# Kernel optimization log

Measured on AMD Instinct MI355X. Metric: run time of the kernel, lower is better.

## Reference

```python
import jax, jax.numpy as jnp
import numpy as np

N = 100000
K = 8
DK = 16          # d_in/K == d_out/K
E = 1600000
EPS = 1e-12      # torch F.normalize eps


def setup_inputs() -> dict:
    key = jax.random.key(0)
    k1, k2, k3, k4 = jax.random.split(key, 4)
    f_in = jax.random.normal(k1, (N, K, DK), dtype=jnp.float32)
    Ep = jax.random.randint(k2, (E, 2), 0, N, dtype=jnp.int64)
    En = jax.random.randint(k3, (E, 2), 0, N, dtype=jnp.int64)
    # xavier_uniform over (K, 5*DK, DK): fan_in=5*DK, fan_out=DK
    limit = float(np.sqrt(6.0 / (5 * DK + DK)))
    W = jax.random.uniform(k4, (K, 5 * DK, DK), dtype=jnp.float32,
                           minval=-limit, maxval=limit)
    b = jnp.zeros((1, K, DK), dtype=jnp.float32)
    return {"f_in": f_in, "Ep": Ep, "En": En, "W": W, "b": b}


def _aggregate(Ep, En, f_in):
    n = f_in.shape[0]
    seg = lambda vals, idx: jax.ops.segment_sum(vals, idx, num_segments=n)
    m_p_out = seg(f_in[Ep[:, 1]], Ep[:, 0])
    m_p_in = seg(f_in[Ep[:, 0]], Ep[:, 1])
    m_n_out = seg(f_in[En[:, 1]], En[:, 0])
    m_n_in = seg(f_in[En[:, 0]], En[:, 1])
    return m_p_out, m_p_in, m_n_out, m_n_in


def reference(f_in, Ep, En, W, b):
    m_p_out, m_p_in, m_n_out, m_n_in = _aggregate(Ep, En, f_in)
    # (N, K, 5*DK)
    m_concat = jnp.concatenate([m_p_out, m_p_in, f_in, m_n_out, m_n_in], axis=2)
    # per-factor grouped matmul: (N,K,5DK) x (K,5DK,DK) -> (N,K,DK)
    f_out = jnp.einsum('nkf,kfo->nko', m_concat, W) + b
    a = jnp.tanh(f_out)
    # F.normalize: L2 over dim=1 (factor axis), clamp_min eps
    norm = jnp.maximum(jnp.linalg.norm(a, axis=1, keepdims=True), EPS)
    return a / norm
```

## Files before the change

kernel.cpp:

```cpp
#include <hip/hip_runtime.h>
#include <math.h>


#define ROW 128
#define ROW4 32
#define BC   256
#define BSH  8

__device__ __forceinline__ void push_entry(
    int* __restrict__ cnt, int* __restrict__ ovfCnt, int* __restrict__ ovf,
    int* __restrict__ idxbuf, int seg, int src, int PAD, int ovfCap)
{
    int slot = atomicAdd(&cnt[seg], 1);
    if (slot < PAD) {
        idxbuf[(size_t)seg * PAD + slot] = src;
    } else {
        int oi = atomicAdd(ovfCnt, 1);
        if (oi < ovfCap) { ovf[2*oi] = seg; ovf[2*oi+1] = src; }
    }
}

__global__ __launch_bounds__(256) void fill_kernel(
    const int4* __restrict__ Ep2, const int4* __restrict__ En2,
    const int* __restrict__ Ep, const int* __restrict__ En,
    int* __restrict__ cnt, int* __restrict__ ovfCnt, int* __restrict__ ovf,
    int* __restrict__ idxbuf, int Epairs, int Etail, int N, int PAD, int ovfCap)
{
    int i = blockIdx.x * 256 + threadIdx.x;
    int stride = gridDim.x * 256;
    for (int e = i; e < Epairs; e += stride) {
        int4 p = Ep2[e];
        push_entry(cnt, ovfCnt, ovf, idxbuf, 4*p.x + 0, p.y, PAD, ovfCap);
        push_entry(cnt, ovfCnt, ovf, idxbuf, 4*p.y + 1, p.x, PAD, ovfCap);
        push_entry(cnt, ovfCnt, ovf, idxbuf, 4*p.z + 0, p.w, PAD, ovfCap);
        push_entry(cnt, ovfCnt, ovf, idxbuf, 4*p.w + 1, p.z, PAD, ovfCap);
        int4 q = En2[e];
        push_entry(cnt, ovfCnt, ovf, idxbuf, 4*q.x + 2, q.y, PAD, ovfCap);
        push_entry(cnt, ovfCnt, ovf, idxbuf, 4*q.y + 3, q.x, PAD, ovfCap);
        push_entry(cnt, ovfCnt, ovf, idxbuf, 4*q.z + 2, q.w, PAD, ovfCap);
        push_entry(cnt, ovfCnt, ovf, idxbuf, 4*q.w + 3, q.z, PAD, ovfCap);
    }
    if (i == 0 && Etail) {
        int e = 2 * Epairs;
        int a = Ep[2*e], b = Ep[2*e+1];
        push_entry(cnt, ovfCnt, ovf, idxbuf, 4*a + 0, b, PAD, ovfCap);
        push_entry(cnt, ovfCnt, ovf, idxbuf, 4*b + 1, a, PAD, ovfCap);
        int c = En[2*e], d = En[2*e+1];
        push_entry(cnt, ovfCnt, ovf, idxbuf, 4*c + 2, d, PAD, ovfCap);
        push_entry(cnt, ovfCnt, ovf, idxbuf, 4*d + 3, c, PAD, ovfCap);
    }
}

__global__ __launch_bounds__(256) void fill_bucket(
    const int4* __restrict__ Ep2, const int4* __restrict__ En2,
    const int* __restrict__ Ep, const int* __restrict__ En,
    int* __restrict__ cnt2, int* __restrict__ cells,
    int* __restrict__ ovfCnt, int* __restrict__ ovf,
    int Epairs, int Etail, int B, int CAP, int ovfCap)
{
    __shared__ int lcnt[1024];
    const int w = blockIdx.x;
    int* __restrict__ mycell = cells + (size_t)w * B * CAP;

    for (int i = threadIdx.x; i < 1024; i += 256) lcnt[i] = 0;
    __syncthreads();

    auto pushB = [&](int dst, int l, int src) {
        int bkt  = dst >> BSH;
        int slot = atomicAdd(&lcnt[bkt], 1);
        if (slot < CAP) {
            mycell[(size_t)bkt * CAP + slot] =
                src | ((dst & (BC - 1)) << 17) | (l << 25);
        } else {
            int oi = atomicAdd(ovfCnt, 1);
            if (oi < ovfCap) { ovf[2*oi] = 4*dst + l; ovf[2*oi+1] = src; }
        }
    };

    int stride = gridDim.x * 256;
    for (int e = blockIdx.x * 256 + threadIdx.x; e < Epairs; e += stride) {
        int4 p = Ep2[e];
        pushB(p.x, 0, p.y); pushB(p.y, 1, p.x);
        pushB(p.z, 0, p.w); pushB(p.w, 1, p.z);
        int4 q = En2[e];
        pushB(q.x, 2, q.y); pushB(q.y, 3, q.x);
        pushB(q.z, 2, q.w); pushB(q.w, 3, q.z);
    }
    if (w == 0 && threadIdx.x == 0 && Etail) {
        int e = 2 * Epairs;
        int a = Ep[2*e], b = Ep[2*e+1];
        pushB(a, 0, b); pushB(b, 1, a);
        int c = En[2*e], d = En[2*e+1];
        pushB(c, 2, d); pushB(d, 3, c);
    }
    __syncthreads();
    for (int b = threadIdx.x; b < B; b += 256) {
        int v = lcnt[b];
        cnt2[(size_t)w * B + b] = (v < CAP) ? v : CAP;
    }
}

__global__ __launch_bounds__(512) void build_csr(
    const int* __restrict__ cnt2, const int* __restrict__ cells,
    int* __restrict__ cnt, int* __restrict__ idxbuf,
    int* __restrict__ ovfCnt, int* __restrict__ ovf,
    int N, int B, int CAP, int PAD, int WN, int ovfCap)
{
    __shared__ int scnt[4 * BC];
    const int b = blockIdx.x;
    const int nodeBase = b << BSH;

    for (int i = threadIdx.x; i < 4 * BC; i += 512) scnt[i] = 0;
    __syncthreads();

    auto proc = [&](int p) {
        int src  = p & 0x1FFFF;
        int dl   = (p >> 17) & (BC - 1);
        int l    = (p >> 25) & 3;
        int segl = (dl << 2) | l;
        int slot = atomicAdd(&scnt[segl], 1);
        if (slot < PAD) {
            idxbuf[(size_t)((nodeBase + dl) * 4 + l) * PAD + slot] = src;
        } else {
            int oi = atomicAdd(ovfCnt, 1);
            if (oi < ovfCap) {
                ovf[2*oi] = (nodeBase + dl) * 4 + l; ovf[2*oi+1] = src;
            }
        }
    };

    for (int w = threadIdx.x; w < WN; w += 512) {
        int c = cnt2[(size_t)w * B + b];
        const int4* __restrict__ cell4 =
            (const int4*)(cells + ((size_t)w * B + b) * CAP);
        for (int i = 0; i < c; i += 4) {
            int4 v = cell4[i >> 2];
            proc(v.x);
            if (i + 1 < c) proc(v.y);
            if (i + 2 < c) proc(v.z);
            if (i + 3 < c) proc(v.w);
        }
    }
    __syncthreads();
    for (int i = threadIdx.x; i < 4 * BC; i += 512) {
        int node = nodeBase + (i >> 2);
        if (node < N) cnt[node * 4 + (i & 3)] = scnt[i];
    }
}

__global__ __launch_bounds__(128) void ovf_zero(
    const int* __restrict__ ovfCnt, const int* __restrict__ ovf,
    float* __restrict__ out, int* __restrict__ nflag, int ovfCap)
{
    const int t = threadIdx.x;
    int nOv = *ovfCnt;
    if (nOv > ovfCap) nOv = ovfCap;
    for (int i = blockIdx.x; i < nOv; i += gridDim.x) {
        int dst = ovf[2*i] >> 2;
        out[(size_t)dst*ROW + t] = 0.f;
        if (t == 0) nflag[dst] = 1;
    }
}

__global__ __launch_bounds__(256) void ovf_kernel(
    const float* __restrict__ f_in, const float* __restrict__ W,
    const int* __restrict__ ovfCnt, const int* __restrict__ ovf,
    float* __restrict__ out, int N, int ovfCap)
{
    const int t = threadIdx.x & 127;
    const int k = t >> 4;
    const int o = t & 15;
    int nOv = *ovfCnt;
    if (nOv > ovfCap) nOv = ovfCap;
    const int group  = blockIdx.x * 2 + (threadIdx.x >> 7);
    const int stride = gridDim.x * 2;
    for (int i = group; i < nOv; i += stride) {
        int seg = ovf[2*i], src = ovf[2*i+1];
        int l = seg & 3;
        int dst = seg >> 2;
        int s = (l < 2) ? l : l + 1;
        float y = 0.f;
#pragma unroll
        for (int ii = 0; ii < 16; ++ii)
            y += f_in[(size_t)src*ROW + k*16 + ii] * W[k*1280 + (s*16 + ii)*16 + o];
        unsafeAtomicAdd(&out[(size_t)dst*ROW + t], y);
    }
}

__global__ __launch_bounds__(256, 4) void pull_kernel(
    const float4* __restrict__ f_in4,
    const float*  __restrict__ f_in,
    const int*    __restrict__ cnt,
    const int*    __restrict__ idxbuf,
    const float*  __restrict__ W,
    const float*  __restrict__ bias,
    const int*    __restrict__ ovfCnt,
    const int*    __restrict__ nflag,
    float*        __restrict__ out,
    int nStart, int nEnd, int PAD)
{
    __shared__ float4 sacc4[2][5][ROW4];
    __shared__ float  syp[2][ROW];
    __shared__ float  sa[ROW];

    const int tid  = threadIdx.x;
    const int elem = tid & 127;
    const int h    = tid >> 7;
    const int k    = elem >> 4;
    const int o    = elem & 15;
    const int oct  = tid >> 5;
    const int l    = oct >> 1;
    const int hh   = oct & 1;
    const int e4   = tid & 31;
    const int slot = (l < 2) ? l : l + 1;

    float w[5][8];
#pragma unroll
    for (int s = 0; s < 5; ++s)
#pragma unroll
        for (int i = 0; i < 8; ++i)
            w[s][i] = W[k*1280 + (s*16 + h*8 + i)*16 + o];
    const float bb = bias[elem];
    const int haveOvf = *ovfCnt;

    for (int n = nStart + blockIdx.x; n < nEnd; n += gridDim.x) {
        float pre = 0.f;
        if (h == 0 && haveOvf)
            pre = nflag[n] ? out[(size_t)n*ROW + elem] : 0.f;

        int c = cnt[4*n + l];
        if (c > PAD) c = PAD;
        const size_t base = (size_t)(4*n + l) * PAD;
        const int mid = (c + 1) >> 1;
        int j         = hh ? mid : 0;
        const int end = hh ? c   : mid;

        float4 acc = make_float4(0.f, 0.f, 0.f, 0.f);
        for (; j + 3 < end; j += 4) {
            int j0 = idxbuf[base + j],     j1 = idxbuf[base + j + 1];
            int j2 = idxbuf[base + j + 2], j3 = idxbuf[base + j + 3];
            float4 r0 = f_in4[(size_t)j0*ROW4 + e4];
            float4 r1 = f_in4[(size_t)j1*ROW4 + e4];
            float4 r2 = f_in4[(size_t)j2*ROW4 + e4];
            float4 r3 = f_in4[(size_t)j3*ROW4 + e4];
            acc.x += r0.x + r1.x + r2.x + r3.x;
            acc.y += r0.y + r1.y + r2.y + r3.y;
            acc.z += r0.z + r1.z + r2.z + r3.z;
            acc.w += r0.w + r1.w + r2.w + r3.w;
        }
        for (; j < end; ++j) {
            float4 r = f_in4[(size_t)idxbuf[base + j]*ROW4 + e4];
            acc.x += r.x; acc.y += r.y; acc.z += r.z; acc.w += r.w;
        }
        sacc4[hh][slot][e4] = acc;
        if (oct == 0) sacc4[0][2][e4] = f_in4[(size_t)n*ROW4 + e4];
        if (oct == 1) sacc4[1][2][e4] = make_float4(0.f, 0.f, 0.f, 0.f);
        __syncthreads();

        float y = 0.f;
#pragma unroll
        for (int s = 0; s < 5; ++s) {
            const float* m0 = (const float*)&sacc4[0][s][0] + k*16 + h*8;
            const float* m1 = (const float*)&sacc4[1][s][0] + k*16 + h*8;
#pragma unroll
            for (int i = 0; i < 8; ++i)
                y += (m0[i] + m1[i]) * w[s][i];
        }
        syp[h][elem] = y;
        __syncthreads();

        float a = 0.f;
        if (h == 0) {
            a = tanhf(syp[0][elem] + syp[1][elem] + bb + pre);
            sa[elem] = a;
        }
        __syncthreads();
        if (h == 0) {
            float ss = 0.f;
#pragma unroll
            for (int k2 = 0; k2 < 8; ++k2) {
                float v = sa[k2*16 + o];
                ss += v * v;
            }
            out[(size_t)n*ROW + elem] = a / fmaxf(sqrtf(ss), 1e-12f);
        }
        __syncthreads();
    }
}

extern "C" void kernel_launch(void* const* d_in, const int* in_sizes, int n_in,
                              void* d_out, int out_size, void* d_ws, size_t ws_size,
                              hipStream_t stream) {
    const float* f_in = (const float*)d_in[0];
    const int*   Ep   = (const int*)d_in[1];
    const int*   En   = (const int*)d_in[2];
    const float* W    = (const float*)d_in[3];
    const float* b    = (const float*)d_in[4];
    float* out = (float*)d_out;

    const int N = in_sizes[0] / ROW;
    const int E = in_sizes[1] / 2;
    const int Epairs = E / 2;
    const int Etail  = E & 1;
    const int M = 4 * N;
    const int B = (N + BC - 1) / BC;
    const int Nh = N >> 1;

    bool newpath = (N <= 131072) && (B <= 1024);
    int PAD = 0, CAP = 0, WN = 0;
    if (newpath) {
        const int cfg1k[][2]  = {{48,32},{40,32},{32,32},{32,24},{24,24},
                                 {24,16},{16,16}};
        const int cfg512[][2] = {{64,48},{48,48},{48,40},{40,40},{40,32},
                                 {32,32},{32,24},{24,24},{16,16}};
        const int wnl[2] = {1024, 512};
        for (int wi = 0; wi < 2 && !WN; ++wi) {
            int wn = wnl[wi];
            const int (*cfg)[2] = wi ? cfg512 : cfg1k;
            int ncfg = wi ? 9 : 7;
            for (int i = 0; i < ncfg; ++i) {
                int pad = cfg[i][0], cap = cfg[i][1];
                size_t need = ((size_t)M + 64 + N + (size_t)wn * B
                               + (size_t)M * pad
                               + (size_t)wn * B * cap) * sizeof(int)
                              + 512 * 1024;
                if (need <= ws_size) { PAD = pad; CAP = cap; WN = wn; break; }
            }
        }
        if (!WN) newpath = false;
    }

    if (newpath) {
        int* cnt    = (int*)d_ws;
        int* ovfCnt = cnt + M;
        int* nflag  = ovfCnt + 64;
        int* cnt2   = nflag + N;
        int* idxbuf = cnt2 + (size_t)WN * B;
        int* cells  = idxbuf + (size_t)M * PAD;
        int* ovf    = cells + (size_t)WN * B * CAP;
        size_t used = ((size_t)M + 64 + N + (size_t)WN * B
                       + (size_t)M * PAD + (size_t)WN * B * CAP) * sizeof(int);
        size_t left = ws_size - used;
        size_t ovfCapSz = left / (2 * sizeof(int));
        int ovfCap = (int)(ovfCapSz > (size_t)(1 << 22) ? (1 << 22) : ovfCapSz);
        if (ovfCap < 1) ovfCap = 1;

        hipMemsetAsync(ovfCnt, 0, ((size_t)64 + N) * sizeof(int), stream);

        fill_bucket<<<WN, 256, 0, stream>>>((const int4*)Ep, (const int4*)En,
                                            Ep, En, cnt2, cells, ovfCnt, ovf,
                                            Epairs, Etail, B, CAP, ovfCap);
        build_csr<<<B, 512, 0, stream>>>(cnt2, cells, cnt, idxbuf,
                                         ovfCnt, ovf, N, B, CAP, PAD, WN,
                                         ovfCap);
        ovf_zero<<<256, 128, 0, stream>>>(ovfCnt, ovf, out, nflag, ovfCap);
        ovf_kernel<<<256, 256, 0, stream>>>(f_in, W, ovfCnt, ovf, out, N,
                                            ovfCap);
        pull_kernel<<<8192, 256, 0, stream>>>((const float4*)f_in, f_in, cnt,
                                              idxbuf, W, b, ovfCnt, nflag,
                                              out, 0, Nh, PAD);
        pull_kernel<<<8192, 256, 0, stream>>>((const float4*)f_in, f_in, cnt,
                                              idxbuf, W, b, ovfCnt, nflag,
                                              out, Nh, N, PAD);
        return;
    }

    int PADf = 72;
    size_t fixed;
    do {
        PADf -= 8;
        fixed = ((size_t)M + 64 + N + (size_t)M * PADf) * sizeof(int);
    } while (PADf > 8 && fixed + 512 * 1024 > ws_size);
    size_t left = (ws_size > fixed) ? (ws_size - fixed) : 8;
    size_t ovfCapSz = left / (2 * sizeof(int));
    int ovfCap = (int)(ovfCapSz > (size_t)(1 << 22) ? (1 << 22) : ovfCapSz);
    if (ovfCap < 1) ovfCap = 1;

    int* cnt    = (int*)d_ws;
    int* ovfCnt = cnt + M;
    int* nflag  = ovfCnt + 64;
    int* idxbuf = nflag + N;
    int* ovf    = idxbuf + (size_t)M * PADf;

    hipMemsetAsync(cnt, 0, ((size_t)M + 64 + N) * sizeof(int), stream);

    fill_kernel<<<2048, 256, 0, stream>>>((const int4*)Ep, (const int4*)En,
                                          Ep, En, cnt, ovfCnt, ovf, idxbuf,
                                          Epairs, Etail, N, PADf, ovfCap);
    ovf_zero<<<256, 128, 0, stream>>>(ovfCnt, ovf, out, nflag, ovfCap);
    ovf_kernel<<<256, 256, 0, stream>>>(f_in, W, ovfCnt, ovf, out, N, ovfCap);
    pull_kernel<<<8192, 256, 0, stream>>>((const float4*)f_in, f_in, cnt,
                                          idxbuf, W, b, ovfCnt, nflag,
                                          out, 0, N, PADf);
}
```

Before: 779.4 us.

## Software-pipeline pull kernel gather with double-buffered shared memory, merge split launches

The pull kernel now prefetches the next node's neighbor gather into registers while it computes the matmul, tanh and normalize for the current node. Shared accumulators are double-buffered, which removes the trailing barrier in each iteration. The two half-range pull launches are merged into one launch over all N. In exchange, register pressure and shared memory use both rise, which may lower occupancy under the launch_bounds(256,4) target.

```diff
diff --git a/kernel.cpp b/kernel.cpp
--- a/kernel.cpp
+++ b/kernel.cpp
@@ -197,9 +197,9 @@
     const int*    __restrict__ ovfCnt,
     const int*    __restrict__ nflag,
     float*        __restrict__ out,
-    int nStart, int nEnd, int PAD)
-{
-    __shared__ float4 sacc4[2][5][ROW4];
+    int N, int PAD)
+{
+    __shared__ float4 sacc4[2][2][5][ROW4];
     __shared__ float  syp[2][ROW];
     __shared__ float  sa[ROW];
 
@@ -223,18 +223,16 @@
     const float bb = bias[elem];
     const int haveOvf = *ovfCnt;
 
-    for (int n = nStart + blockIdx.x; n < nEnd; n += gridDim.x) {
-        float pre = 0.f;
-        if (h == 0 && haveOvf)
-            pre = nflag[n] ? out[(size_t)n*ROW + elem] : 0.f;
-
-        int c = cnt[4*n + l];
+    float4 racc  = make_float4(0.f, 0.f, 0.f, 0.f);
+    float4 rself = make_float4(0.f, 0.f, 0.f, 0.f);
+
+    auto do_gather = [&](int node) {
+        int c = cnt[4*node + l];
         if (c > PAD) c = PAD;
-        const size_t base = (size_t)(4*n + l) * PAD;
+        const size_t base = (size_t)(4*node + l) * PAD;
         const int mid = (c + 1) >> 1;
         int j         = hh ? mid : 0;
         const int end = hh ? c   : mid;
-
         float4 acc = make_float4(0.f, 0.f, 0.f, 0.f);
         for (; j + 3 < end; j += 4) {
             int j0 = idxbuf[base + j],     j1 = idxbuf[base + j + 1];
@@ -252,16 +250,35 @@
             float4 r = f_in4[(size_t)idxbuf[base + j]*ROW4 + e4];
             acc.x += r.x; acc.y += r.y; acc.z += r.z; acc.w += r.w;
         }
-        sacc4[hh][slot][e4] = acc;
-        if (oct == 0) sacc4[0][2][e4] = f_in4[(size_t)n*ROW4 + e4];
-        if (oct == 1) sacc4[1][2][e4] = make_float4(0.f, 0.f, 0.f, 0.f);
+        racc = acc;
+        if (oct == 0) rself = f_in4[(size_t)node*ROW4 + e4];
+    };
+
+    if (oct == 1) {
+        sacc4[0][1][2][e4] = make_float4(0.f, 0.f, 0.f, 0.f);
+        sacc4[1][1][2][e4] = make_float4(0.f, 0.f, 0.f, 0.f);
+    }
+
+    int n = blockIdx.x;
+    if (n < N) do_gather(n);
+    int cur = 0;
+
+    for (; n < N; n += gridDim.x) {
+        sacc4[cur][hh][slot][e4] = racc;
+        if (oct == 0) sacc4[cur][0][2][e4] = rself;
+        float pre = 0.f;
+        if (h == 0 && haveOvf)
+            pre = nflag[n] ? out[(size_t)n*ROW + elem] : 0.f;
         __syncthreads();
 
+        int nn = n + gridDim.x;
+        if (nn < N) do_gather(nn);
+
         float y = 0.f;
 #pragma unroll
         for (int s = 0; s < 5; ++s) {
-            const float* m0 = (const float*)&sacc4[0][s][0] + k*16 + h*8;
-            const float* m1 = (const float*)&sacc4[1][s][0] + k*16 + h*8;
+            const float* m0 = (const float*)&sacc4[cur][0][s][0] + k*16 + h*8;
+            const float* m1 = (const float*)&sacc4[cur][1][s][0] + k*16 + h*8;
 #pragma unroll
             for (int i = 0; i < 8; ++i)
                 y += (m0[i] + m1[i]) * w[s][i];
@@ -269,12 +286,12 @@
         syp[h][elem] = y;
         __syncthreads();
 
-        float a = 0.f;
         if (h == 0) {
-            a = tanhf(syp[0][elem] + syp[1][elem] + bb + pre);
+            float a = tanhf(syp[0][elem] + syp[1][elem] + bb + pre);
             sa[elem] = a;
         }
         __syncthreads();
+
         if (h == 0) {
             float ss = 0.f;
 #pragma unroll
@@ -282,9 +299,9 @@
                 float v = sa[k2*16 + o];
                 ss += v * v;
             }
-            out[(size_t)n*ROW + elem] = a / fmaxf(sqrtf(ss), 1e-12f);
-        }
-        __syncthreads();
+            out[(size_t)n*ROW + elem] = sa[elem] / fmaxf(sqrtf(ss), 1e-12f);
+        }
+        cur ^= 1;
     }
 }
 
@@ -304,7 +321,6 @@
     const int Etail  = E & 1;
     const int M = 4 * N;
     const int B = (N + BC - 1) / BC;
-    const int Nh = N >> 1;
 
     bool newpath = (N <= 131072) && (B <= 1024);
     int PAD = 0, CAP = 0, WN = 0;
@@ -358,10 +374,7 @@
                                             ovfCap);
         pull_kernel<<<8192, 256, 0, stream>>>((const float4*)f_in, f_in, cnt,
                                               idxbuf, W, b, ovfCnt, nflag,
-                                              out, 0, Nh, PAD);
-        pull_kernel<<<8192, 256, 0, stream>>>((const float4*)f_in, f_in, cnt,
-                                              idxbuf, W, b, ovfCnt, nflag,
-                                              out, Nh, N, PAD);
+                                              out, N, PAD);
         return;
     }
 
@@ -391,5 +404,5 @@
     ovf_kernel<<<256, 256, 0, stream>>>(f_in, W, ovfCnt, ovf, out, N, ovfCap);
     pull_kernel<<<8192, 256, 0, stream>>>((const float4*)f_in, f_in, cnt,
                                           idxbuf, W, b, ovfCnt, nflag,
-                                          out, 0, N, PADf);
-}
+                                          out, N, PADf);
+}
```

New measurement: 806.9 us. +3.5%, slower.
